# Performance work log

Measured on AMD Instinct MI355X. Metric: run time of the kernel, lower is better.

## Reference

```python
import jax, jax.numpy as jnp
import numpy as np

DIM = 1024
NUM_HEADS = 16
HEAD_DIM = DIM // NUM_HEADS
ROPE_THETA = 10000.0
SCALE = HEAD_DIM ** -0.5


def _apply_rope(x, cos, sin):
    # x: [B, H, S, head_dim]; cos/sin: [S, head_dim//2] (broadcast over B, H)
    x_even = x[..., 0::2]
    x_odd = x[..., 1::2]
    rot_even = x_even * cos - x_odd * sin
    rot_odd = x_even * sin + x_odd * cos
    # interleave back: stack on last axis then flatten, matching torch .stack(-1).flatten(-2)
    return jnp.stack([rot_even, rot_odd], axis=-1).reshape(x.shape)


def setup_inputs() -> dict:
    key = jax.random.key(0)
    k0, k1, k2 = jax.random.split(key, 3)
    B, S = 2, 2048
    x = jax.random.normal(k0, (B, S, DIM), dtype=jnp.float32)
    # small_init: std = sqrt(2 / (5*dim))
    qkv_w = jax.random.normal(k1, (3 * DIM, DIM), dtype=jnp.float32) * (2.0 / (5 * DIM)) ** 0.5
    qkv_b = jnp.zeros((3 * DIM,), dtype=jnp.float32)
    # wang_init: std = 2 / num_blocks / sqrt(dim) scaled
    out_w = jax.random.normal(k2, (DIM, DIM), dtype=jnp.float32) * (2.0 / DIM) ** 0.5 / 2.0
    out_b = jnp.zeros((DIM,), dtype=jnp.float32)
    return {"x": x, "qkv_w": qkv_w, "qkv_b": qkv_b, "out_w": out_w, "out_b": out_b, "window_size": 512}


def reference(x, qkv_w, qkv_b, out_w, out_b, window_size):
    B, S, D = x.shape
    qkv = x @ qkv_w.T + qkv_b                          # [B, S, 3D]
    qkv = qkv.reshape(B, S, 3, NUM_HEADS, HEAD_DIM).transpose(2, 0, 3, 1, 4)
    q, k, v = qkv[0], qkv[1], qkv[2]                   # each [B, H, S, hd]

    pos = jnp.arange(S, dtype=jnp.float32)
    inv_freq = 1.0 / (ROPE_THETA ** (jnp.arange(0, HEAD_DIM, 2, dtype=jnp.float32) / HEAD_DIM))
    freqs = pos[:, None] * inv_freq                    # [S, hd//2]
    cos, sin = jnp.cos(freqs), jnp.sin(freqs)
    q = _apply_rope(q, cos, sin)
    k = _apply_rope(k, cos, sin)

    scores = jnp.einsum('bhqd,bhkd->bhqk', q, k) * SCALE
    i = jnp.arange(S)
    mask = (i[:, None] >= i[None, :]) & ((i[:, None] - i[None, :]) < window_size)  # causal sliding window
    scores = jnp.where(mask, scores, -jnp.inf)
    attn = jax.nn.softmax(scores, axis=-1)
    out = jnp.einsum('bhqk,bhkd->bhqd', attn, v)       # [B, H, S, hd]
    out = out.transpose(0, 2, 1, 3).reshape(B, S, D)
    return out @ out_w.T + out_b
```

## Files before the change

### kernel.cpp

```cpp
#include <hip/hip_runtime.h>
#include <hip/hip_bf16.h>
#include <cstdint>
#include <cstddef>

using bf16x8 = __attribute__((ext_vector_type(8))) short;
using f32x4  = __attribute__((ext_vector_type(4))) float;

#define MFMA16(a, b, c) __builtin_amdgcn_mfma_f32_16x16x32_bf16((a), (b), (c), 0, 0, 0)

__device__ __forceinline__ unsigned short f2bf(float f) {
    unsigned int u = __float_as_uint(f);
    u += 0x7fffu + ((u >> 16) & 1u);
    return (unsigned short)(u >> 16);
}
__device__ __forceinline__ uint32_t pack2bf(float a, float b) {
    __hip_bfloat162 h = __float22bfloat162_rn(float2{a, b});
    return *(uint32_t*)&h;
}
__device__ __forceinline__ float bf2f(short x) {
    return __uint_as_float(((uint32_t)(unsigned short)x) << 16);
}
__device__ __forceinline__ float bflo(uint32_t p) { return __uint_as_float(p << 16); }
__device__ __forceinline__ float bfhi(uint32_t p) { return __uint_as_float(p & 0xffff0000u); }

__device__ __forceinline__ void gload_lds16(const void* g, void* l) {
    __builtin_amdgcn_global_load_lds(
        (const __attribute__((address_space(1))) void*)g,
        (__attribute__((address_space(3))) void*)l, 16, 0, 0);
}

#define S_LEN 2048
#define NHEAD 16
#define HDIM  64
#define DIM   1024
#define WIN   512
#define MROWS 4096

__global__ void prep(float* __restrict__ cosT, float* __restrict__ sinT,
                     const float* __restrict__ x, unsigned short* __restrict__ xb,
                     const float* __restrict__ qw, unsigned short* __restrict__ qwb,
                     const float* __restrict__ ow, unsigned short* __restrict__ owb) {
    int t = blockIdx.x * 256 + threadIdx.x;
    if (t < 65536) {
        int s = t >> 5, f = t & 31;
        float invf = powf(10000.0f, -(float)f / 32.0f);
        float ang = (float)s * invf;
        cosT[t] = cosf(ang);
        sinT[t] = sinf(ang);
        return;
    }
    int u = t - 65536;
    const float* src;
    unsigned short* dst;
    int i;
    if (u < 1048576)        { src = x;  dst = xb;  i = u * 4; }
    else if (u < 1835008)   { src = qw; dst = qwb; i = (u - 1048576) * 4; }
    else                    { src = ow; dst = owb; i = (u - 1835008) * 4; }
    float4 v = *(const float4*)(src + i);
    ushort4 o;
    o.x = f2bf(v.x); o.y = f2bf(v.y); o.z = f2bf(v.z); o.w = f2bf(v.w);
    *(ushort4*)(dst + i) = o;
}


__global__ __launch_bounds__(256) void gemm_qkv_fused(
        const unsigned short* __restrict__ A,
        const unsigned short* __restrict__ Bw,
        const float* __restrict__ bias,
        const float* __restrict__ cosT, const float* __restrict__ sinT,
        unsigned short* __restrict__ qbuf,
        unsigned short* __restrict__ kbuf,
        unsigned short* __restrict__ vtb) {
    __shared__ __align__(16) char smem_raw[32768];
    const int tid = threadIdx.x;
    const int lane = tid & 63, w = tid >> 6;
    const int wr = w >> 1, wc = w & 1, lm = lane & 15, lg = lane >> 4;
    const int bx = blockIdx.x, by = blockIdx.y;
    const int row0 = by * 128, col0 = bx * 128;
    const int plane = bx >> 3;
    const int h0 = (bx & 7) * 2;
    const int b = by >> 4, s_base = (by & 15) * 128;

    f32x4 acc[4][4];
#pragma unroll
    for (int m = 0; m < 4; ++m)
#pragma unroll
        for (int n = 0; n < 4; ++n) acc[m][n] = (f32x4){0.f, 0.f, 0.f, 0.f};

    auto As = [&](int buf) { return (short*)(smem_raw + buf * 16384); };
    auto Bs = [&](int buf) { return (short*)(smem_raw + buf * 16384 + 8192); };

    const size_t ldb = 2048;
    auto stage = [&](int kt, int buf) {
#pragma unroll
        for (int i = 0; i < 2; ++i) {
            int c = tid + 256 * i;
            int r = c >> 2, gp = c & 3;
            int gs = gp ^ ((r >> 1) & 3);
            gload_lds16((const char*)A  + (size_t)(row0 + r) * ldb + (size_t)kt * 64 + gs * 16, As(buf) + c * 8);
            gload_lds16((const char*)Bw + (size_t)(col0 + r) * ldb + (size_t)kt * 64 + gs * 16, Bs(buf) + c * 8);
        }
    };

    stage(0, 0);
    __syncthreads();
    int cur = 0;
    const int swz = (lm >> 1) & 3;
    for (int kt = 0; kt < 32; ++kt) {
        if (kt + 1 < 32) stage(kt + 1, cur ^ 1);
        bf16x8 af[4], bfr[4];
        const short* as = As(cur);
        const short* bs = Bs(cur);
#pragma unroll
        for (int m = 0; m < 4; ++m) af[m]  = *(const bf16x8*)&as[(wr * 64 + m * 16 + lm) * 32 + ((lg ^ swz) << 3)];
#pragma unroll
        for (int n = 0; n < 4; ++n) bfr[n] = *(const bf16x8*)&bs[(wc * 64 + n * 16 + lm) * 32 + ((lg ^ swz) << 3)];
#pragma unroll
        for (int m = 0; m < 4; ++m)
#pragma unroll
            for (int n = 0; n < 4; ++n) acc[m][n] = MFMA16(af[m], bfr[n], acc[m][n]);
        __syncthreads();
        cur ^= 1;
    }

    unsigned short (*tile)[136] = (unsigned short(*)[136])smem_raw;
    unsigned short (*tileT)[72] = (unsigned short(*)[72])smem_raw;
    const int lane8 = tid & 7, idx = tid >> 3;

#pragma unroll 1
    for (int half = 0; half < 2; ++half) {
        __syncthreads();
        if (wr == half) {
            if (plane < 2) {
#pragma unroll
                for (int m = 0; m < 4; ++m)
#pragma unroll
                    for (int n = 0; n < 4; ++n) {
                        int colL = wc * 64 + n * 16 + lm;
                        float bv = bias[col0 + colL];
#pragma unroll
                        for (int r = 0; r < 4; ++r)
                            tile[m * 16 + lg * 4 + r][colL] = f2bf(acc[m][n][r] + bv);
                    }
            } else {
#pragma unroll
                for (int m = 0; m < 4; ++m)
#pragma unroll
                    for (int n = 0; n < 4; ++n) {
                        int colL = wc * 64 + n * 16 + lm;
                        float bv = bias[col0 + colL];
                        uint2 pk;
                        pk.x = pack2bf(acc[m][n][0] + bv, acc[m][n][1] + bv);
                        pk.y = pack2bf(acc[m][n][2] + bv, acc[m][n][3] + bv);
                        *(uint2*)&tileT[colL][m * 16 + lg * 4] = pk;
                    }
            }
        }
        __syncthreads();
        if (plane < 2) {
            unsigned short* dstp = (plane == 0) ? qbuf : kbuf;
            const float qsc = (plane == 0) ? 0.125f : 1.0f;
            int d0 = lane8 * 8;
#pragma unroll
            for (int j = 0; j < 2; ++j) {
                int srow = idx + 32 * j;
                int s = s_base + half * 64 + srow;
                float4 c4 = *(const float4*)&cosT[s * 32 + (d0 >> 1)];
                float4 s4 = *(const float4*)&sinT[s * 32 + (d0 >> 1)];
#pragma unroll
                for (int hh = 0; hh < 2; ++hh) {
                    bf16x8 v = *(const bf16x8*)&tile[srow][hh * 64 + d0];
                    float e0 = bf2f(v[0]), o0 = bf2f(v[1]);
                    float e1 = bf2f(v[2]), o1 = bf2f(v[3]);
                    float e2 = bf2f(v[4]), o2 = bf2f(v[5]);
                    float e3 = bf2f(v[6]), o3 = bf2f(v[7]);
                    uint4 pk;
                    pk.x = pack2bf((e0 * c4.x - o0 * s4.x) * qsc, (e0 * s4.x + o0 * c4.x) * qsc);
                    pk.y = pack2bf((e1 * c4.y - o1 * s4.y) * qsc, (e1 * s4.y + o1 * c4.y) * qsc);
                    pk.z = pack2bf((e2 * c4.z - o2 * s4.z) * qsc, (e2 * s4.z + o2 * c4.z) * qsc);
                    pk.w = pack2bf((e3 * c4.w - o3 * s4.w) * qsc, (e3 * s4.w + o3 * c4.w) * qsc);
                    int h = h0 + hh;
                    *(uint4*)&dstp[(((size_t)(b * NHEAD + h)) * S_LEN + s) * 64 + d0] = pk;
                }
            }
        } else {
#pragma unroll
            for (int rr = 0; rr < 4; ++rr) {
                int hd = rr * 32 + idx;
                int hh = hd >> 6, d = hd & 63, h = h0 + hh;
                bf16x8 v = *(const bf16x8*)&tileT[hd][lane8 * 8];
                *(bf16x8*)&vtb[((size_t)(b * NHEAD + h) * 64 + d) * S_LEN +
                               s_base + half * 64 + lane8 * 8] = v;
            }
        }
    }
}

__global__ __launch_bounds__(256) void gemm_out(const unsigned short* __restrict__ A,
                                                const unsigned short* __restrict__ Bw,
                                                const float* __restrict__ bias,
                                                float* __restrict__ Cout) {
    __shared__ __align__(16) char smem_raw[32768];
    const int tid = threadIdx.x;
    const int lane = tid & 63, w = tid >> 6;
    const int wr = w >> 1, wc = w & 1, lm = lane & 15, lg = lane >> 4;
    const int row0 = blockIdx.y * 128, col0 = blockIdx.x * 128;

    f32x4 acc[4][4];
#pragma unroll
    for (int m = 0; m < 4; ++m)
#pragma unroll
        for (int n = 0; n < 4; ++n) acc[m][n] = (f32x4){0.f, 0.f, 0.f, 0.f};

    auto As = [&](int buf) { return (short*)(smem_raw + buf * 16384); };
    auto Bs = [&](int buf) { return (short*)(smem_raw + buf * 16384 + 8192); };

    const size_t ldb = 2048;
    auto stage = [&](int kt, int buf) {
#pragma unroll
        for (int i = 0; i < 2; ++i) {
            int c = tid + 256 * i;
            int r = c >> 2, gp = c & 3;
            int gs = gp ^ ((r >> 1) & 3);
            gload_lds16((const char*)A  + (size_t)(row0 + r) * ldb + (size_t)kt * 64 + gs * 16, As(buf) + c * 8);
            gload_lds16((const char*)Bw + (size_t)(col0 + r) * ldb + (size_t)kt * 64 + gs * 16, Bs(buf) + c * 8);
        }
    };

    stage(0, 0);
    __syncthreads();
    int cur = 0;
    const int swz = (lm >> 1) & 3;
    for (int kt = 0; kt < 32; ++kt) {
        if (kt + 1 < 32) stage(kt + 1, cur ^ 1);
        bf16x8 af[4], bfr[4];
        const short* as = As(cur);
        const short* bs = Bs(cur);
#pragma unroll
        for (int m = 0; m < 4; ++m) af[m]  = *(const bf16x8*)&as[(wr * 64 + m * 16 + lm) * 32 + ((lg ^ swz) << 3)];
#pragma unroll
        for (int n = 0; n < 4; ++n) bfr[n] = *(const bf16x8*)&bs[(wc * 64 + n * 16 + lm) * 32 + ((lg ^ swz) << 3)];
#pragma unroll
        for (int m = 0; m < 4; ++m)
#pragma unroll
            for (int n = 0; n < 4; ++n) acc[m][n] = MFMA16(af[m], bfr[n], acc[m][n]);
        __syncthreads();
        cur ^= 1;
    }

#pragma unroll
    for (int m = 0; m < 4; ++m) {
        int row = row0 + wr * 64 + m * 16 + lg * 4;
#pragma unroll
        for (int n = 0; n < 4; ++n) {
            int col = col0 + wc * 64 + n * 16 + lm;
            float bv = bias[col];
#pragma unroll
            for (int r = 0; r < 4; ++r)
                Cout[(size_t)(row + r) * DIM + col] = acc[m][n][r] + bv;
        }
    }
}

__global__ __launch_bounds__(256) void attn(const unsigned short* __restrict__ qb,
                                            const unsigned short* __restrict__ kb,
                                            const unsigned short* __restrict__ vt,
                                            unsigned short* __restrict__ ao) {
    const int p = blockIdx.x;
    const int L = (p & 7) * 128 + (p >> 3);
    const int qblk = L & 31, bh = L >> 5;
    const int b = bh >> 4, h = bh & 15;
    const int tid = threadIdx.x, w = tid >> 6, lane = tid & 63;
    const int lm = lane & 15, lg = lane >> 4;
    const unsigned short* Qb = qb + (size_t)bh * S_LEN * 64;
    const unsigned short* Kb = kb + (size_t)bh * S_LEN * 64;
    const unsigned short* Vt = vt + (size_t)bh * 64 * S_LEN;
    const int q0 = qblk * 64 + w * 16;

    __shared__ short Ks[2][64 * 64];
    __shared__ short Vs[2][64 * 64];
    __shared__ short Plds[4][16 * 64];
    short* Pw = Plds[w];

    bf16x8 aq0 = *(const bf16x8*)&Qb[(q0 + lm) * 64 + lg * 8];
    bf16x8 aq1 = *(const bf16x8*)&Qb[(q0 + lm) * 64 + lg * 8 + 32];

    f32x4 o[4];
#pragma unroll
    for (int n = 0; n < 4; ++n) o[n] = (f32x4){0.f, 0.f, 0.f, 0.f};
    float lsum = 0.f;

    const int qq = q0 + lm;
    const int t0 = qblk >= 8 ? qblk - 8 : 0;

    auto stage = [&](int kt, int buf) {
#pragma unroll
        for (int i = 0; i < 2; ++i) {
            int c = tid + 256 * i;
            int r = c >> 3, g = (c & 7) ^ (r & 7);
            gload_lds16(Kb + (size_t)(kt * 64 + r) * 64 + g * 8, &Ks[buf][c * 8]);
            gload_lds16(Vt + (size_t)r * S_LEN + kt * 64 + g * 8, &Vs[buf][c * 8]);
        }
    };

    stage(t0, 0);
    __syncthreads();
    int cur = 0;
    for (int kt = t0; kt <= qblk; ++kt) {
        if (kt < qblk) stage(kt + 1, cur ^ 1);
        const int kbase = kt * 64;
        const int sw = lm & 7;
        f32x4 sT[4];
#pragma unroll
        for (int n = 0; n < 4; ++n) {
            int rl = n * 16 + lm;
            bf16x8 bk0 = *(const bf16x8*)&Ks[cur][rl * 64 + ((lg ^ sw) << 3)];
            bf16x8 bk1 = *(const bf16x8*)&Ks[cur][rl * 64 + (((lg + 4) ^ sw) << 3)];
            f32x4 z = (f32x4){0.f, 0.f, 0.f, 0.f};
            z = MFMA16(bk0, aq0, z);
            sT[n] = MFMA16(bk1, aq1, z);
        }
#pragma unroll
        for (int n = 0; n < 4; ++n) {
            int kk0 = kbase + n * 16 + lg * 4;
#pragma unroll
            for (int r = 0; r < 4; ++r) {
                int d = qq - (kk0 + r);
                float sv = ((unsigned)d < (unsigned)WIN) ? sT[n][r] : -1e30f;
                float pv = __expf(sv);
                sT[n][r] = pv;
                lsum += pv;
            }
            uint2 pk;
            pk.x = pack2bf(sT[n][0], sT[n][1]);
            pk.y = pack2bf(sT[n][2], sT[n][3]);
            *(uint2*)&Pw[lm * 64 + ((((2 * n + (lg >> 1)) ^ sw) << 3) + ((lg & 1) << 2))] = pk;
        }
        bf16x8 ap0 = *(const bf16x8*)&Pw[lm * 64 + ((lg ^ sw) << 3)];
        bf16x8 ap1 = *(const bf16x8*)&Pw[lm * 64 + (((lg + 4) ^ sw) << 3)];
#pragma unroll
        for (int n = 0; n < 4; ++n) {
            int rl = n * 16 + lm;
            bf16x8 bv0 = *(const bf16x8*)&Vs[cur][rl * 64 + ((lg ^ sw) << 3)];
            bf16x8 bv1 = *(const bf16x8*)&Vs[cur][rl * 64 + (((lg + 4) ^ sw) << 3)];
            o[n] = MFMA16(ap0, bv0, o[n]);
            o[n] = MFMA16(ap1, bv1, o[n]);
        }
        __syncthreads();
        cur ^= 1;
    }
    lsum += __shfl_xor(lsum, 16, 64);
    lsum += __shfl_xor(lsum, 32, 64);
    float linv = 1.f / lsum;
    float lrow[4];
#pragma unroll
    for (int r = 0; r < 4; ++r) lrow[r] = __shfl(linv, lg * 4 + r, 64);
#pragma unroll
    for (int n = 0; n < 4; ++n)
#pragma unroll
        for (int r = 0; r < 4; ++r) {
            int row = b * S_LEN + q0 + lg * 4 + r;
            int col = h * 64 + n * 16 + lm;
            ao[(size_t)row * DIM + col] = f2bf(o[n][r] * lrow[r]);
        }
}

extern "C" void kernel_launch(void* const* d_in, const int* in_sizes, int n_in,
                              void* d_out, int out_size, void* d_ws, size_t ws_size,
                              hipStream_t stream) {
    const float* x      = (const float*)d_in[0];
    const float* qkv_w  = (const float*)d_in[1];
    const float* qkv_b  = (const float*)d_in[2];
    const float* out_w  = (const float*)d_in[3];
    const float* out_b  = (const float*)d_in[4];
    (void)in_sizes; (void)n_in; (void)out_size; (void)ws_size;

    char* ws = (char*)d_ws;
    float*          cosT = (float*)(ws + 0);
    float*          sinT = (float*)(ws + 262144);
    unsigned short* xb   = (unsigned short*)(ws + 524288);
    unsigned short* wqb  = (unsigned short*)(ws + 8912896);
    unsigned short* owb  = (unsigned short*)(ws + 15204352);
    unsigned short* qbuf = (unsigned short*)(ws + 17301504);
    unsigned short* kbuf = (unsigned short*)(ws + 25690112);
    unsigned short* vtb  = (unsigned short*)(ws + 34078720);
    unsigned short* aob  = (unsigned short*)(ws + 42467328);

    prep<<<8448, 256, 0, stream>>>(cosT, sinT, x, xb, qkv_w, wqb, out_w, owb);

    gemm_qkv_fused<<<dim3(24, 32), 256, 0, stream>>>(xb, wqb, qkv_b, cosT, sinT,
                                                     qbuf, kbuf, vtb);

    attn<<<1024, 256, 0, stream>>>(qbuf, kbuf, vtb, aob);

    gemm_out<<<dim3(8, 32), 256, 0, stream>>>(aob, owb, out_b, (float*)d_out);
}
```

Before: 105.0 us.

## Double query rows per attention block and single-pass QKV epilogue

The attention kernel now assigns 128 query rows per block (32 per wave, two MFMA row tiles), so each staged K/V tile is reused across twice as many queries and the grid is halved. Masked entries skip the exp and contribute zero. The QKV GEMM epilogue writes the whole 128x128 tile to a larger shared buffer in one pass instead of two halves, which removes a sync round. The cost is higher register use and LDS in attention, fewer blocks for occupancy, and extra key tiles per block because the sliding-window span now covers 128 queries.

```diff
diff --git a/kernel.cpp b/kernel.cpp
--- a/kernel.cpp
+++ b/kernel.cpp
@@ -20,8 +20,6 @@
 __device__ __forceinline__ float bf2f(short x) {
     return __uint_as_float(((uint32_t)(unsigned short)x) << 16);
 }
-__device__ __forceinline__ float bflo(uint32_t p) { return __uint_as_float(p << 16); }
-__device__ __forceinline__ float bfhi(uint32_t p) { return __uint_as_float(p & 0xffff0000u); }
 
 __device__ __forceinline__ void gload_lds16(const void* g, void* l) {
     __builtin_amdgcn_global_load_lds(
@@ -62,7 +60,6 @@
     *(ushort4*)(dst + i) = o;
 }
 
-
 __global__ __launch_bounds__(256) void gemm_qkv_fused(
         const unsigned short* __restrict__ A,
         const unsigned short* __restrict__ Bw,
@@ -71,7 +68,7 @@
         unsigned short* __restrict__ qbuf,
         unsigned short* __restrict__ kbuf,
         unsigned short* __restrict__ vtb) {
-    __shared__ __align__(16) char smem_raw[32768];
+    __shared__ __align__(16) char smem_raw[34816];
     const int tid = threadIdx.x;
     const int lane = tid & 63, w = tid >> 6;
     const int wr = w >> 1, wc = w & 1, lm = lane & 15, lg = lane >> 4;
@@ -124,73 +121,71 @@
     }
 
     unsigned short (*tile)[136] = (unsigned short(*)[136])smem_raw;
-    unsigned short (*tileT)[72] = (unsigned short(*)[72])smem_raw;
     const int lane8 = tid & 7, idx = tid >> 3;
 
-#pragma unroll 1
-    for (int half = 0; half < 2; ++half) {
-        __syncthreads();
-        if (wr == half) {
-            if (plane < 2) {
-#pragma unroll
-                for (int m = 0; m < 4; ++m)
-#pragma unroll
-                    for (int n = 0; n < 4; ++n) {
-                        int colL = wc * 64 + n * 16 + lm;
-                        float bv = bias[col0 + colL];
-#pragma unroll
-                        for (int r = 0; r < 4; ++r)
-                            tile[m * 16 + lg * 4 + r][colL] = f2bf(acc[m][n][r] + bv);
-                    }
-            } else {
-#pragma unroll
-                for (int m = 0; m < 4; ++m)
-#pragma unroll
-                    for (int n = 0; n < 4; ++n) {
-                        int colL = wc * 64 + n * 16 + lm;
-                        float bv = bias[col0 + colL];
-                        uint2 pk;
-                        pk.x = pack2bf(acc[m][n][0] + bv, acc[m][n][1] + bv);
-                        pk.y = pack2bf(acc[m][n][2] + bv, acc[m][n][3] + bv);
-                        *(uint2*)&tileT[colL][m * 16 + lg * 4] = pk;
-                    }
-            }
-        }
-        __syncthreads();
-        if (plane < 2) {
-            unsigned short* dstp = (plane == 0) ? qbuf : kbuf;
-            const float qsc = (plane == 0) ? 0.125f : 1.0f;
-            int d0 = lane8 * 8;
+    if (plane < 2) {
+#pragma unroll
+        for (int m = 0; m < 4; ++m)
+#pragma unroll
+            for (int n = 0; n < 4; ++n) {
+                int colL = wc * 64 + n * 16 + lm;
+                float bv = bias[col0 + colL];
+#pragma unroll
+                for (int r = 0; r < 4; ++r)
+                    tile[wr * 64 + m * 16 + lg * 4 + r][colL] = f2bf(acc[m][n][r] + bv);
+            }
+    } else {
+#pragma unroll
+        for (int m = 0; m < 4; ++m)
+#pragma unroll
+            for (int n = 0; n < 4; ++n) {
+                int colL = wc * 64 + n * 16 + lm;
+                float bv = bias[col0 + colL];
+                uint2 pk;
+                pk.x = pack2bf(acc[m][n][0] + bv, acc[m][n][1] + bv);
+                pk.y = pack2bf(acc[m][n][2] + bv, acc[m][n][3] + bv);
+                *(uint2*)&tile[colL][wr * 64 + m * 16 + lg * 4] = pk;
+            }
+    }
+    __syncthreads();
+
+    if (plane < 2) {
+        unsigned short* dstp = (plane == 0) ? qbuf : kbuf;
+        const float qsc = (plane == 0) ? 0.125f : 1.0f;
+        int d0 = lane8 * 8;
+#pragma unroll
+        for (int j = 0; j < 4; ++j) {
+            int srow = idx + 32 * j;
+            int s = s_base + srow;
+            float4 c4 = *(const float4*)&cosT[s * 32 + (d0 >> 1)];
+            float4 s4 = *(const float4*)&sinT[s * 32 + (d0 >> 1)];
+#pragma unroll
+            for (int hh = 0; hh < 2; ++hh) {
+                bf16x8 v = *(const bf16x8*)&tile[srow][hh * 64 + d0];
+                float e0 = bf2f(v[0]), o0 = bf2f(v[1]);
+                float e1 = bf2f(v[2]), o1 = bf2f(v[3]);
+                float e2 = bf2f(v[4]), o2 = bf2f(v[5]);
+                float e3 = bf2f(v[6]), o3 = bf2f(v[7]);
+                uint4 pk;
+                pk.x = pack2bf((e0 * c4.x - o0 * s4.x) * qsc, (e0 * s4.x + o0 * c4.x) * qsc);
+                pk.y = pack2bf((e1 * c4.y - o1 * s4.y) * qsc, (e1 * s4.y + o1 * c4.y) * qsc);
+                pk.z = pack2bf((e2 * c4.z - o2 * s4.z) * qsc, (e2 * s4.z + o2 * c4.z) * qsc);
+                pk.w = pack2bf((e3 * c4.w - o3 * s4.w) * qsc, (e3 * s4.w + o3 * c4.w) * qsc);
+                int h = h0 + hh;
+                *(uint4*)&dstp[(((size_t)(b * NHEAD + h)) * S_LEN + s) * 64 + d0] = pk;
+            }
+        }
+    } else {
+#pragma unroll
+        for (int rr = 0; rr < 4; ++rr) {
+            int hd = rr * 32 + idx;
+            int hh = hd >> 6, d = hd & 63, h = h0 + hh;
 #pragma unroll
             for (int j = 0; j < 2; ++j) {
-                int srow = idx + 32 * j;
-                int s = s_base + half * 64 + srow;
-                float4 c4 = *(const float4*)&cosT[s * 32 + (d0 >> 1)];
-                float4 s4 = *(const float4*)&sinT[s * 32 + (d0 >> 1)];
-#pragma unroll
-                for (int hh = 0; hh < 2; ++hh) {
-                    bf16x8 v = *(const bf16x8*)&tile[srow][hh * 64 + d0];
-                    float e0 = bf2f(v[0]), o0 = bf2f(v[1]);
-                    float e1 = bf2f(v[2]), o1 = bf2f(v[3]);
-                    float e2 = bf2f(v[4]), o2 = bf2f(v[5]);
-                    float e3 = bf2f(v[6]), o3 = bf2f(v[7]);
-                    uint4 pk;
-                    pk.x = pack2bf((e0 * c4.x - o0 * s4.x) * qsc, (e0 * s4.x + o0 * c4.x) * qsc);
-                    pk.y = pack2bf((e1 * c4.y - o1 * s4.y) * qsc, (e1 * s4.y + o1 * c4.y) * qsc);
-                    pk.z = pack2bf((e2 * c4.z - o2 * s4.z) * qsc, (e2 * s4.z + o2 * c4.z) * qsc);
-                    pk.w = pack2bf((e3 * c4.w - o3 * s4.w) * qsc, (e3 * s4.w + o3 * c4.w) * qsc);
-                    int h = h0 + hh;
-                    *(uint4*)&dstp[(((size_t)(b * NHEAD + h)) * S_LEN + s) * 64 + d0] = pk;
-                }
-            }
-        } else {
-#pragma unroll
-            for (int rr = 0; rr < 4; ++rr) {
-                int hd = rr * 32 + idx;
-                int hh = hd >> 6, d = hd & 63, h = h0 + hh;
-                bf16x8 v = *(const bf16x8*)&tileT[hd][lane8 * 8];
+                int s0 = lane8 * 8 + j * 64;
+                bf16x8 v = *(const bf16x8*)&tile[hd][s0];
                 *(bf16x8*)&vtb[((size_t)(b * NHEAD + h) * 64 + d) * S_LEN +
-                               s_base + half * 64 + lane8 * 8] = v;
+                               s_base + s0] = v;
             }
         }
     }
@@ -267,31 +262,37 @@
                                             const unsigned short* __restrict__ vt,
                                             unsigned short* __restrict__ ao) {
     const int p = blockIdx.x;
-    const int L = (p & 7) * 128 + (p >> 3);
-    const int qblk = L & 31, bh = L >> 5;
+    const int L = (p & 7) * 64 + (p >> 3);
+    const int qbk = L & 15, bh = L >> 4;
     const int b = bh >> 4, h = bh & 15;
     const int tid = threadIdx.x, w = tid >> 6, lane = tid & 63;
     const int lm = lane & 15, lg = lane >> 4;
     const unsigned short* Qb = qb + (size_t)bh * S_LEN * 64;
     const unsigned short* Kb = kb + (size_t)bh * S_LEN * 64;
     const unsigned short* Vt = vt + (size_t)bh * 64 * S_LEN;
-    const int q0 = qblk * 64 + w * 16;
+    const int q0w = qbk * 128 + w * 32;
 
     __shared__ short Ks[2][64 * 64];
     __shared__ short Vs[2][64 * 64];
-    __shared__ short Plds[4][16 * 64];
+    __shared__ short Plds[4][32 * 64];
     short* Pw = Plds[w];
 
-    bf16x8 aq0 = *(const bf16x8*)&Qb[(q0 + lm) * 64 + lg * 8];
-    bf16x8 aq1 = *(const bf16x8*)&Qb[(q0 + lm) * 64 + lg * 8 + 32];
-
-    f32x4 o[4];
-#pragma unroll
-    for (int n = 0; n < 4; ++n) o[n] = (f32x4){0.f, 0.f, 0.f, 0.f};
-    float lsum = 0.f;
-
-    const int qq = q0 + lm;
-    const int t0 = qblk >= 8 ? qblk - 8 : 0;
+    bf16x8 aq[2][2];
+#pragma unroll
+    for (int mi = 0; mi < 2; ++mi) {
+        aq[mi][0] = *(const bf16x8*)&Qb[(q0w + mi * 16 + lm) * 64 + lg * 8];
+        aq[mi][1] = *(const bf16x8*)&Qb[(q0w + mi * 16 + lm) * 64 + lg * 8 + 32];
+    }
+
+    f32x4 o[2][4];
+#pragma unroll
+    for (int mi = 0; mi < 2; ++mi)
+#pragma unroll
+        for (int n = 0; n < 4; ++n) o[mi][n] = (f32x4){0.f, 0.f, 0.f, 0.f};
+    float lsum0 = 0.f, lsum1 = 0.f;
+
+    const int t0 = (qbk >= 4) ? (2 * qbk - 8) : 0;
+    const int t1 = 2 * qbk + 1;
 
     auto stage = [&](int kt, int buf) {
 #pragma unroll
@@ -306,63 +307,82 @@
     stage(t0, 0);
     __syncthreads();
     int cur = 0;
-    for (int kt = t0; kt <= qblk; ++kt) {
-        if (kt < qblk) stage(kt + 1, cur ^ 1);
+    const int sw = lm & 7;
+    for (int kt = t0; kt <= t1; ++kt) {
+        if (kt < t1) stage(kt + 1, cur ^ 1);
         const int kbase = kt * 64;
-        const int sw = lm & 7;
-        f32x4 sT[4];
+        f32x4 sT[2][4];
 #pragma unroll
         for (int n = 0; n < 4; ++n) {
             int rl = n * 16 + lm;
             bf16x8 bk0 = *(const bf16x8*)&Ks[cur][rl * 64 + ((lg ^ sw) << 3)];
             bf16x8 bk1 = *(const bf16x8*)&Ks[cur][rl * 64 + (((lg + 4) ^ sw) << 3)];
-            f32x4 z = (f32x4){0.f, 0.f, 0.f, 0.f};
-            z = MFMA16(bk0, aq0, z);
-            sT[n] = MFMA16(bk1, aq1, z);
-        }
-#pragma unroll
-        for (int n = 0; n < 4; ++n) {
-            int kk0 = kbase + n * 16 + lg * 4;
-#pragma unroll
-            for (int r = 0; r < 4; ++r) {
-                int d = qq - (kk0 + r);
-                float sv = ((unsigned)d < (unsigned)WIN) ? sT[n][r] : -1e30f;
-                float pv = __expf(sv);
-                sT[n][r] = pv;
-                lsum += pv;
-            }
-            uint2 pk;
-            pk.x = pack2bf(sT[n][0], sT[n][1]);
-            pk.y = pack2bf(sT[n][2], sT[n][3]);
-            *(uint2*)&Pw[lm * 64 + ((((2 * n + (lg >> 1)) ^ sw) << 3) + ((lg & 1) << 2))] = pk;
-        }
-        bf16x8 ap0 = *(const bf16x8*)&Pw[lm * 64 + ((lg ^ sw) << 3)];
-        bf16x8 ap1 = *(const bf16x8*)&Pw[lm * 64 + (((lg + 4) ^ sw) << 3)];
+#pragma unroll
+            for (int mi = 0; mi < 2; ++mi) {
+                f32x4 z = (f32x4){0.f, 0.f, 0.f, 0.f};
+                z = MFMA16(bk0, aq[mi][0], z);
+                sT[mi][n] = MFMA16(bk1, aq[mi][1], z);
+            }
+        }
+#pragma unroll
+        for (int mi = 0; mi < 2; ++mi) {
+            const int qq = q0w + mi * 16 + lm;
+#pragma unroll
+            for (int n = 0; n < 4; ++n) {
+                int kk0 = kbase + n * 16 + lg * 4;
+#pragma unroll
+                for (int r = 0; r < 4; ++r) {
+                    int d = qq - (kk0 + r);
+                    float pv = ((unsigned)d < (unsigned)WIN) ? __expf(sT[mi][n][r]) : 0.f;
+                    sT[mi][n][r] = pv;
+                    if (mi == 0) lsum0 += pv; else lsum1 += pv;
+                }
+                uint2 pk;
+                pk.x = pack2bf(sT[mi][n][0], sT[mi][n][1]);
+                pk.y = pack2bf(sT[mi][n][2], sT[mi][n][3]);
+                *(uint2*)&Pw[(mi * 16 + lm) * 64 +
+                             ((((2 * n + (lg >> 1)) ^ sw) << 3) + ((lg & 1) << 2))] = pk;
+            }
+        }
+        bf16x8 ap[2][2];
+#pragma unroll
+        for (int mi = 0; mi < 2; ++mi) {
+            ap[mi][0] = *(const bf16x8*)&Pw[(mi * 16 + lm) * 64 + ((lg ^ sw) << 3)];
+            ap[mi][1] = *(const bf16x8*)&Pw[(mi * 16 + lm) * 64 + (((lg + 4) ^ sw) << 3)];
+        }
 #pragma unroll
         for (int n = 0; n < 4; ++n) {
             int rl = n * 16 + lm;
             bf16x8 bv0 = *(const bf16x8*)&Vs[cur][rl * 64 + ((lg ^ sw) << 3)];
             bf16x8 bv1 = *(const bf16x8*)&Vs[cur][rl * 64 + (((lg + 4) ^ sw) << 3)];
-            o[n] = MFMA16(ap0, bv0, o[n]);
-            o[n] = MFMA16(ap1, bv1, o[n]);
+#pragma unroll
+            for (int mi = 0; mi < 2; ++mi) {
+                o[mi][n] = MFMA16(ap[mi][0], bv0, o[mi][n]);
+                o[mi][n] = MFMA16(ap[mi][1], bv1, o[mi][n]);
+            }
         }
         __syncthreads();
         cur ^= 1;
     }
-    lsum += __shfl_xor(lsum, 16, 64);
-    lsum += __shfl_xor(lsum, 32, 64);
-    float linv = 1.f / lsum;
-    float lrow[4];
-#pragma unroll
-    for (int r = 0; r < 4; ++r) lrow[r] = __shfl(linv, lg * 4 + r, 64);
-#pragma unroll
-    for (int n = 0; n < 4; ++n)
+    lsum0 += __shfl_xor(lsum0, 16, 64);
+    lsum0 += __shfl_xor(lsum0, 32, 64);
+    lsum1 += __shfl_xor(lsum1, 16, 64);
+    lsum1 += __shfl_xor(lsum1, 32, 64);
+    float linv0 = 1.f / lsum0, linv1 = 1.f / lsum1;
+#pragma unroll
+    for (int mi = 0; mi < 2; ++mi) {
+        float lv = (mi == 0) ? linv0 : linv1;
 #pragma unroll
         for (int r = 0; r < 4; ++r) {
-            int row = b * S_LEN + q0 + lg * 4 + r;
-            int col = h * 64 + n * 16 + lm;
-            ao[(size_t)row * DIM + col] = f2bf(o[n][r] * lrow[r]);
-        }
+            float lr = __shfl(lv, lg * 4 + r, 64);
+            int row = b * S_LEN + q0w + mi * 16 + lg * 4 + r;
+#pragma unroll
+            for (int n = 0; n < 4; ++n) {
+                int col = h * 64 + n * 16 + lm;
+                ao[(size_t)row * DIM + col] = f2bf(o[mi][n][r] * lr);
+            }
+        }
+    }
 }
 
 extern "C" void kernel_launch(void* const* d_in, const int* in_sizes, int n_in,
@@ -391,7 +411,7 @@
     gemm_qkv_fused<<<dim3(24, 32), 256, 0, stream>>>(xb, wqb, qkv_b, cosT, sinT,
                                                      qbuf, kbuf, vtb);
 
-    attn<<<1024, 256, 0, stream>>>(qbuf, kbuf, vtb, aob);
+    attn<<<512, 256, 0, stream>>>(qbuf, kbuf, vtb, aob);
 
     gemm_out<<<dim3(8, 32), 256, 0, stream>>>(aob, owb, out_b, (float*)d_out);
 }
```

New measurement: 105.9 us. No clear change (+0.9%).
